# Kernel tuning notes

Hardware: AMD Instinct MI355X
Metric: run time of the kernel (lower is better)

## Reference

```python
import jax, jax.numpy as jnp
import numpy as np

HIDDEN = 256
B, L = 4, 4096


def setup_inputs() -> dict:
    key = jax.random.key(0)
    k_in, k_q, k_k, k_v, k_len = jax.random.split(key, 5)
    inputs = jax.random.normal(k_in, (B, L, HIDDEN), dtype=jnp.float32)
    # torch.rand -> uniform [0,1)
    W_query = jax.random.uniform(k_q, (HIDDEN, HIDDEN), dtype=jnp.float32)
    W_key = jax.random.uniform(k_k, (HIDDEN, HIDDEN), dtype=jnp.float32)
    W_value = jax.random.uniform(k_v, (HIDDEN, HIDDEN), dtype=jnp.float32)
    lengths = jax.random.randint(k_len, (B,), 1, L + 1, dtype=jnp.int64)
    return {"inputs": inputs, "W_query": W_query, "W_key": W_key,
            "W_value": W_value, "lengths": lengths}


def reference(inputs, W_query, W_key, W_value, lengths):
    # lengths is unused by the original module (no masking applied).
    # QKV projections (batched matmul with shared weight)
    queries = jnp.einsum('blh,hd->bld', inputs, W_query)
    keys = jnp.einsum('blh,hd->bld', inputs, W_key)
    values = jnp.einsum('blh,hd->bld', inputs, W_value)
    # scaled dot-product attention, full [B, L, L] scores as in original
    scale = 1.0 / jnp.sqrt(jnp.asarray(HIDDEN, dtype=inputs.dtype))
    attn_scores = jnp.einsum('bqd,bkd->bqk', queries, keys) * scale
    attentions = jax.nn.softmax(attn_scores, axis=-1)
    weighted = jnp.einsum('bqk,bkd->bqd', attentions, values)
    return weighted
```

## Files before the change

### kernel.cpp

```cpp
#include <hip/hip_runtime.h>


typedef __bf16 bf16x8 __attribute__((ext_vector_type(8)));
typedef _Float16 f16x8 __attribute__((ext_vector_type(8)));
typedef _Float16 f16x4 __attribute__((ext_vector_type(4)));
typedef float floatx4 __attribute__((ext_vector_type(4)));

#define MFMA16B(a, b, c) __builtin_amdgcn_mfma_f32_16x16x32_bf16(a, b, c, 0, 0, 0)
#define MFMA16F(a, b, c) __builtin_amdgcn_mfma_f32_16x16x32_f16(a, b, c, 0, 0, 0)
#define GLOAD_LDS16(g, l)                                                  \
  __builtin_amdgcn_global_load_lds(                                        \
      (const __attribute__((address_space(1))) void *)(g),                 \
      (__attribute__((address_space(3))) void *)(l), 16, 0, 0)

#define HID 256
#define LSEQ 4096
#define NB 4
#define NTOK (NB * LSEQ)
#define PLANE ((size_t)NTOK * HID)
#define NSPLIT 4
#define QSCALE 0.09016844005556021f


__device__ __forceinline__ void split_bf16(float v, __bf16 &h, __bf16 &l) {
  h = (__bf16)v;
  l = (__bf16)(v - (float)h);
}

__global__ __launch_bounds__(256) void wsplit(const float *__restrict__ Wq,
                                              const float *__restrict__ Wk,
                                              const float *__restrict__ Wv,
                                              __bf16 *__restrict__ Wht,
                                              __bf16 *__restrict__ Wlt) {
  __shared__ float tile[32][256];
  const int wsel = blockIdx.x;
  const int hb = blockIdx.y;
  const float *W = (wsel == 0) ? Wq : (wsel == 1) ? Wk : Wv;
  __bf16 *oh = Wht + wsel * HID * HID;
  __bf16 *ol = Wlt + wsel * HID * HID;
  const int t = threadIdx.x;
  #pragma unroll
  for (int p = 0; p < 8; ++p) {
    int r = p * 4 + (t >> 6);
    int c = (t & 63) * 4;
    *(floatx4 *)&tile[r][c] = *(const floatx4 *)&W[(hb * 32 + r) * HID + c];
  }
  __syncthreads();
  #pragma unroll
  for (int q = 0; q < 4; ++q) {
    int n = q * 64 + (t >> 2);
    int hs = (t & 3) * 8;
    bf16x8 hh, ll;
    #pragma unroll
    for (int i = 0; i < 8; ++i) {
      float v = tile[hs + i][n];
      __bf16 h, l;
      split_bf16(v, h, l);
      hh[i] = h; ll[i] = l;
    }
    *(bf16x8 *)&oh[n * HID + hb * 32 + hs] = hh;
    *(bf16x8 *)&ol[n * HID + hb * 32 + hs] = ll;
  }
}

__global__ __launch_bounds__(256, 2) void qkv_proj(const float *__restrict__ X,
                                                   const __bf16 *__restrict__ Wht,
                                                   const __bf16 *__restrict__ Wlt,
                                                   _Float16 *__restrict__ Qf,
                                                   _Float16 *__restrict__ Kf,
                                                   _Float16 *__restrict__ Vf) {
  __shared__ __bf16 WhS[64 * 256];
  __shared__ __bf16 WlS[64 * 256];
  _Float16 *Tf = (_Float16 *)WhS;

  const int mtile = blockIdx.x;
  const int col0 = blockIdx.y * 64;
  const int tid = threadIdx.x;
  const int w4 = tid >> 6;
  const int lane = tid & 63;
  const int quad = lane >> 4;
  const int ln = lane & 15;
  const int arow = mtile * 64 + w4 * 16 + ln;

  bf16x8 ah[8], al[8];
  #pragma unroll
  for (int kc = 0; kc < 8; ++kc) {
    const float *xp = X + (size_t)arow * HID + kc * 32 + quad * 8;
    floatx4 x0 = *(const floatx4 *)xp;
    floatx4 x1 = *(const floatx4 *)(xp + 4);
    #pragma unroll
    for (int j = 0; j < 4; ++j) {
      __bf16 h, l;
      split_bf16(x0[j], h, l); ah[kc][j] = h; al[kc][j] = l;
      split_bf16(x1[j], h, l); ah[kc][4 + j] = h; al[kc][4 + j] = l;
    }
  }

  const int srow = tid >> 2;
  const int sseg = tid & 3;

  bf16x8 pwh[8], pwl[8];
  {
    const size_t wbase = (size_t)(col0 + srow) * HID;
    #pragma unroll
    for (int j = 0; j < 8; ++j) {
      const int chunk = j * 4 + sseg;
      pwh[j] = *(const bf16x8 *)&Wht[wbase + chunk * 8];
      pwl[j] = *(const bf16x8 *)&Wlt[wbase + chunk * 8];
    }
  }

  for (int w = 0; w < 3; ++w) {
    __syncthreads();
    #pragma unroll
    for (int j = 0; j < 8; ++j) {
      const int chunk = j * 4 + sseg;
      const int dst = srow * 256 + ((chunk ^ (srow & 7)) << 3);
      *(bf16x8 *)&WhS[dst] = pwh[j];
      if (w < 2) *(bf16x8 *)&WlS[dst] = pwl[j];
    }
    __syncthreads();

    if (w < 2) {
      const size_t wbase = (size_t)(w + 1) * HID * HID + (size_t)(col0 + srow) * HID;
      #pragma unroll
      for (int j = 0; j < 8; ++j) {
        const int chunk = j * 4 + sseg;
        pwh[j] = *(const bf16x8 *)&Wht[wbase + chunk * 8];
        pwl[j] = *(const bf16x8 *)&Wlt[wbase + chunk * 8];
      }
    }

    floatx4 acc[4] = {};
    #pragma unroll
    for (int kc = 0; kc < 8; ++kc) {
      #pragma unroll
      for (int nt = 0; nt < 4; ++nt) {
        const int a = (nt * 16 + ln) * 256 + (((kc * 4 + quad) ^ (ln & 7)) << 3);
        bf16x8 bh = *(const bf16x8 *)&WhS[a];
        acc[nt] = MFMA16B(ah[kc], bh, acc[nt]);
        if (w < 2) {
          bf16x8 bl = *(const bf16x8 *)&WlS[a];
          acc[nt] = MFMA16B(ah[kc], bl, acc[nt]);
        }
        acc[nt] = MFMA16B(al[kc], bh, acc[nt]);
      }
    }

    if (w == 0) {
      #pragma unroll
      for (int nt = 0; nt < 4; ++nt) {
        #pragma unroll
        for (int r = 0; r < 4; ++r) {
          const int orow = mtile * 64 + w4 * 16 + quad * 4 + r;
          const int ocol = col0 + nt * 16 + ln;
          Qf[(size_t)orow * HID + ocol] = (_Float16)(acc[nt][r] * QSCALE);
        }
      }
    } else if (w == 1) {
      __syncthreads();
      #pragma unroll
      for (int nt = 0; nt < 4; ++nt) {
        #pragma unroll
        for (int r = 0; r < 4; ++r) {
          const int tok_l = w4 * 16 + quad * 4 + r;
          const int h_l = nt * 16 + ln;
          Tf[tok_l * 72 + h_l] = (_Float16)acc[nt][r];
        }
      }
      __syncthreads();
      #pragma unroll
      for (int i = 0; i < 2; ++i) {
        const int c = i * 256 + tid;
        const int lane_f = c & 63;
        const int ntf = (c >> 6) & 1;
        const int kcL = (c >> 7) & 1;
        const int t2 = (c >> 8) & 1;
        const int qf = lane_f >> 4;
        const int lnf = lane_f & 15;
        const int tok_l = t2 * 32 + ntf * 16 + lnf;
        f16x8 v = *(const f16x8 *)&Tf[tok_l * 72 + kcL * 32 + qf * 8];
        const int T = mtile * 2 + t2;
        const int kc = (col0 >> 5) + kcL;
        *(f16x8 *)&Kf[(size_t)T * 8192 + ((ntf * 8 + kc) * 64 + lane_f) * 8] = v;
      }
    } else {
      __syncthreads();
      #pragma unroll
      for (int nt = 0; nt < 4; ++nt) {
        #pragma unroll
        for (int r = 0; r < 4; ++r) {
          const int tok_l = w4 * 16 + quad * 4 + r;
          const int d_l = nt * 16 + ln;
          Tf[d_l * 72 + tok_l] = (_Float16)acc[nt][r];
        }
      }
      __syncthreads();
      #pragma unroll
      for (int i = 0; i < 2; ++i) {
        const int c = i * 256 + tid;
        const int lane_f = c & 63;
        const int dtL = (c >> 6) & 3;
        const int t2 = (c >> 8) & 1;
        const int qf = lane_f >> 4;
        const int lnf = lane_f & 15;
        const int d_l = dtL * 16 + lnf;
        f16x4 lo = *(const f16x4 *)&Tf[d_l * 72 + t2 * 32 + 4 * qf];
        f16x4 hi = *(const f16x4 *)&Tf[d_l * 72 + t2 * 32 + 16 + 4 * qf];
        f16x8 v;
        v[0] = lo[0]; v[1] = lo[1]; v[2] = lo[2]; v[3] = lo[3];
        v[4] = hi[0]; v[5] = hi[1]; v[6] = hi[2]; v[7] = hi[3];
        const int T = mtile * 2 + t2;
        const int dt = (col0 >> 4) + dtL;
        *(f16x8 *)&Vf[(size_t)(T * 16 + dt) * 512 + lane_f * 8] = v;
      }
    }
  }
}

__global__ __launch_bounds__(256, 2) void attn(const _Float16 *__restrict__ Qf,
                                               const _Float16 *__restrict__ Kf,
                                               const _Float16 *__restrict__ Vf,
                                               _Float16 *__restrict__ Op,
                                               float *__restrict__ Mp,
                                               float *__restrict__ Lp) {
  __shared__ _Float16 KS[2][8192];
  __shared__ _Float16 VS[2][8192];

  const int bx = blockIdx.x;
  const int ks = bx & 3;
  const int qt = bx >> 2;
  const int b = qt >> 5;
  const int qtl = qt & 31;
  const int tid = threadIdx.x;
  const int w4 = tid >> 6;
  const int lane = tid & 63;
  const int quad = lane >> 4;
  const int ln = lane & 15;
  const int T0 = b * 128 + ks * 32;

  const int qtok0 = b * LSEQ + qtl * 128 + w4 * 16 + ln;
  const int qtok1 = qtok0 + 64;
  f16x8 q0[8], q1[8];
  #pragma unroll
  for (int kc = 0; kc < 8; ++kc) {
    q0[kc] = *(const f16x8 *)&Qf[(size_t)qtok0 * HID + kc * 32 + quad * 8];
    q1[kc] = *(const f16x8 *)&Qf[(size_t)qtok1 * HID + kc * 32 + quad * 8];
  }

  const _Float16 *kuni = Kf + (size_t)T0 * 8192;
  const _Float16 *vuni = Vf + (size_t)T0 * 8192;
  const int koff = tid * 8;
  const int voff = lane * 8;

  #pragma unroll
  for (int i = 0; i < 4; ++i)
    GLOAD_LDS16(kuni + i * 2048 + koff, &KS[0][i * 2048 + koff]);
  #pragma unroll
  for (int i = 0; i < 4; ++i)
    GLOAD_LDS16(vuni + i * 2048 + koff, &VS[0][i * 2048 + koff]);

  float m0 = -1e30f, m1 = -1e30f;
  float l0 = 0.f, l1 = 0.f;
  floatx4 o0[16] = {}, o1[16] = {};

  for (int t = 0; t < 32; ++t) {
    const int buf = t & 1;
    asm volatile("s_waitcnt vmcnt(0)" ::: "memory");
    __builtin_amdgcn_s_barrier();
    __builtin_amdgcn_sched_barrier(0);
    if (t < 31) {
      const _Float16 *ksrc = kuni + (size_t)(t + 1) * 8192 + koff;
      const _Float16 *vsrc = vuni + (size_t)(t + 1) * 8192 + koff;
      #pragma unroll
      for (int i = 0; i < 4; ++i)
        GLOAD_LDS16(ksrc + i * 2048, &KS[buf ^ 1][i * 2048 + koff]);
      #pragma unroll
      for (int i = 0; i < 4; ++i)
        GLOAD_LDS16(vsrc + i * 2048, &VS[buf ^ 1][i * 2048 + koff]);
    }
    const _Float16 *Kb = KS[buf];
    const _Float16 *Vb = VS[buf];

    floatx4 s00, s01, s10, s11;
    {
      floatx4 a00 = {}, b00 = {}, a01 = {}, b01 = {};
      floatx4 a10 = {}, b10 = {}, a11 = {}, b11 = {};
      __builtin_amdgcn_s_setprio(1);
      #pragma unroll
      for (int kc = 0; kc < 4; ++kc) {
        const f16x8 k0 = *(const f16x8 *)(Kb + kc * 512 + voff);
        const f16x8 k1 = *(const f16x8 *)(Kb + (4 + kc) * 512 + voff);
        const f16x8 k2 = *(const f16x8 *)(Kb + (8 + kc) * 512 + voff);
        const f16x8 k3 = *(const f16x8 *)(Kb + (12 + kc) * 512 + voff);
        a00 = MFMA16F(k0, q0[kc], a00);
        a10 = MFMA16F(k0, q1[kc], a10);
        b00 = MFMA16F(k1, q0[4 + kc], b00);
        b10 = MFMA16F(k1, q1[4 + kc], b10);
        a01 = MFMA16F(k2, q0[kc], a01);
        a11 = MFMA16F(k2, q1[kc], a11);
        b01 = MFMA16F(k3, q0[4 + kc], b01);
        b11 = MFMA16F(k3, q1[4 + kc], b11);
      }
      __builtin_amdgcn_s_setprio(0);
      s00 = a00 + b00; s01 = a01 + b01;
      s10 = a10 + b10; s11 = a11 + b11;
    }

    float al0, al1;
    {
      float tmax = fmaxf(fmaxf(fmaxf(s00[0], s00[1]), fmaxf(s00[2], s00[3])),
                         fmaxf(fmaxf(s01[0], s01[1]), fmaxf(s01[2], s01[3])));
      tmax = fmaxf(tmax, __shfl_xor(tmax, 16));
      tmax = fmaxf(tmax, __shfl_xor(tmax, 32));
      const float mn = fmaxf(m0, tmax);
      al0 = exp2f(m0 - mn);
      #pragma unroll
      for (int i = 0; i < 4; ++i) {
        s00[i] = exp2f(s00[i] - mn);
        s01[i] = exp2f(s01[i] - mn);
      }
      float rs = ((s00[0] + s00[1]) + (s00[2] + s00[3])) +
                 ((s01[0] + s01[1]) + (s01[2] + s01[3]));
      rs += __shfl_xor(rs, 16);
      rs += __shfl_xor(rs, 32);
      l0 = l0 * al0 + rs;
      m0 = mn;
    }
    {
      float tmax = fmaxf(fmaxf(fmaxf(s10[0], s10[1]), fmaxf(s10[2], s10[3])),
                         fmaxf(fmaxf(s11[0], s11[1]), fmaxf(s11[2], s11[3])));
      tmax = fmaxf(tmax, __shfl_xor(tmax, 16));
      tmax = fmaxf(tmax, __shfl_xor(tmax, 32));
      const float mn = fmaxf(m1, tmax);
      al1 = exp2f(m1 - mn);
      #pragma unroll
      for (int i = 0; i < 4; ++i) {
        s10[i] = exp2f(s10[i] - mn);
        s11[i] = exp2f(s11[i] - mn);
      }
      float rs = ((s10[0] + s10[1]) + (s10[2] + s10[3])) +
                 ((s11[0] + s11[1]) + (s11[2] + s11[3]));
      rs += __shfl_xor(rs, 16);
      rs += __shfl_xor(rs, 32);
      l1 = l1 * al1 + rs;
      m1 = mn;
    }

    f16x8 pf0, pf1;
    pf0[0] = (_Float16)s00[0]; pf0[1] = (_Float16)s00[1];
    pf0[2] = (_Float16)s00[2]; pf0[3] = (_Float16)s00[3];
    pf0[4] = (_Float16)s01[0]; pf0[5] = (_Float16)s01[1];
    pf0[6] = (_Float16)s01[2]; pf0[7] = (_Float16)s01[3];
    pf1[0] = (_Float16)s10[0]; pf1[1] = (_Float16)s10[1];
    pf1[2] = (_Float16)s10[2]; pf1[3] = (_Float16)s10[3];
    pf1[4] = (_Float16)s11[0]; pf1[5] = (_Float16)s11[1];
    pf1[6] = (_Float16)s11[2]; pf1[7] = (_Float16)s11[3];

    if (__any(al0 < 1.0f)) {
      #pragma unroll
      for (int dt = 0; dt < 16; ++dt) {
        o0[dt][0] *= al0; o0[dt][1] *= al0; o0[dt][2] *= al0; o0[dt][3] *= al0;
      }
    }
    if (__any(al1 < 1.0f)) {
      #pragma unroll
      for (int dt = 0; dt < 16; ++dt) {
        o1[dt][0] *= al1; o1[dt][1] *= al1; o1[dt][2] *= al1; o1[dt][3] *= al1;
      }
    }

    __builtin_amdgcn_s_setprio(1);
    #pragma unroll
    for (int dt = 0; dt < 16; ++dt) {
      const f16x8 vf = *(const f16x8 *)(Vb + dt * 512 + voff);
      o0[dt] = MFMA16F(vf, pf0, o0[dt]);
      o1[dt] = MFMA16F(vf, pf1, o1[dt]);
    }
    __builtin_amdgcn_s_setprio(0);
    __builtin_amdgcn_sched_barrier(0);
  }

  #pragma unroll
  for (int dt = 0; dt < 16; ++dt) {
    f16x4 v4;
    v4[0] = (_Float16)o0[dt][0]; v4[1] = (_Float16)o0[dt][1];
    v4[2] = (_Float16)o0[dt][2]; v4[3] = (_Float16)o0[dt][3];
    *(f16x4 *)&Op[(size_t)ks * PLANE + (size_t)qtok0 * HID + dt * 16 + quad * 4] = v4;
    f16x4 w4v;
    w4v[0] = (_Float16)o1[dt][0]; w4v[1] = (_Float16)o1[dt][1];
    w4v[2] = (_Float16)o1[dt][2]; w4v[3] = (_Float16)o1[dt][3];
    *(f16x4 *)&Op[(size_t)ks * PLANE + (size_t)qtok1 * HID + dt * 16 + quad * 4] = w4v;
  }
  if (quad == 0) {
    Mp[ks * NTOK + qtok0] = m0;
    Lp[ks * NTOK + qtok0] = l0;
    Mp[ks * NTOK + qtok1] = m1;
    Lp[ks * NTOK + qtok1] = l1;
  }
}

__global__ __launch_bounds__(256) void merge(const _Float16 *__restrict__ Op,
                                             const float *__restrict__ Mp,
                                             const float *__restrict__ Lp,
                                             float *__restrict__ Out) {
  const int row = blockIdx.x * 4 + (threadIdx.x >> 6);
  const int c = (threadIdx.x & 63) * 4;
  float ms[NSPLIT], ls[NSPLIT];
  #pragma unroll
  for (int s = 0; s < NSPLIT; ++s) {
    ms[s] = Mp[s * NTOK + row];
    ls[s] = Lp[s * NTOK + row];
  }
  const float M = fmaxf(fmaxf(ms[0], ms[1]), fmaxf(ms[2], ms[3]));
  float e[NSPLIT], den = 0.f;
  #pragma unroll
  for (int s = 0; s < NSPLIT; ++s) {
    e[s] = exp2f(ms[s] - M);
    den += ls[s] * e[s];
  }
  const float inv = 1.0f / den;
  floatx4 out = {};
  #pragma unroll
  for (int s = 0; s < NSPLIT; ++s) {
    const f16x4 a = *(const f16x4 *)&Op[(size_t)s * PLANE + (size_t)row * HID + c];
    const float w = e[s] * inv;
    #pragma unroll
    for (int i = 0; i < 4; ++i) out[i] += w * (float)a[i];
  }
  *(floatx4 *)&Out[(size_t)row * HID + c] = out;
}

extern "C" void kernel_launch(void *const *d_in, const int *in_sizes, int n_in,
                              void *d_out, int out_size, void *d_ws, size_t ws_size,
                              hipStream_t stream) {
  const float *X = (const float *)d_in[0];
  const float *Wq = (const float *)d_in[1];
  const float *Wk = (const float *)d_in[2];
  const float *Wv = (const float *)d_in[3];

  _Float16 *ws = (_Float16 *)d_ws;
  _Float16 *Qf = ws;
  _Float16 *Kf = Qf + PLANE;
  _Float16 *Vf = Kf + PLANE;
  __bf16 *Wht = (__bf16 *)(Vf + PLANE);
  __bf16 *Wlt = Wht + 3 * HID * HID;
  _Float16 *Op = (_Float16 *)(Wlt + 3 * HID * HID);
  float *Mp = (float *)(Op + NSPLIT * PLANE);
  float *Lp = Mp + NSPLIT * NTOK;

  wsplit<<<dim3(3, 8), 256, 0, stream>>>(Wq, Wk, Wv, Wht, Wlt);
  qkv_proj<<<dim3(256, 4), 256, 0, stream>>>(X, Wht, Wlt, Qf, Kf, Vf);
  attn<<<NTOK / 128 * NSPLIT, 256, 0, stream>>>(Qf, Kf, Vf, Op, Mp, Lp);
  merge<<<NTOK / 4, 256, 0, stream>>>(Op, Mp, Lp, (float *)d_out);
}
```

Measured before the change: 206.7 us.

## Process 128 rows per block in QKV projection to reuse staged weights

Each qkv_proj block now handles two 64-row token tiles, so every weight tile staged in shared memory feeds twice as many MFMAs, and the grid is halved. The register prefetch of the next weight matrix is dropped in favor of loading each matrix at the top of its loop iteration. The transpose buffer gets its own shared allocation, raising LDS use to about 73 KB and register pressure from doubled A fragments and accumulators, which may hurt occupancy under the launch bound of 2. The projection is a small part of total time next to attention.

After: 202.3 us. 1.02x faster.

```diff
diff --git a/kernel.cpp b/kernel.cpp
--- a/kernel.cpp
+++ b/kernel.cpp
@@ -71,7 +71,7 @@
                                                    _Float16 *__restrict__ Vf) {
   __shared__ __bf16 WhS[64 * 256];
   __shared__ __bf16 WlS[64 * 256];
-  _Float16 *Tf = (_Float16 *)WhS;
+  __shared__ _Float16 Tf[64 * 72];
 
   const int mtile = blockIdx.x;
   const int col0 = blockIdx.y * 64;
@@ -80,70 +80,76 @@
   const int lane = tid & 63;
   const int quad = lane >> 4;
   const int ln = lane & 15;
-  const int arow = mtile * 64 + w4 * 16 + ln;
-
-  bf16x8 ah[8], al[8];
+  const int arow0 = mtile * 128 + w4 * 16 + ln;
+  const int arow1 = arow0 + 64;
+
+  bf16x8 ah0[8], al0[8], ah1[8], al1[8];
   #pragma unroll
   for (int kc = 0; kc < 8; ++kc) {
-    const float *xp = X + (size_t)arow * HID + kc * 32 + quad * 8;
-    floatx4 x0 = *(const floatx4 *)xp;
-    floatx4 x1 = *(const floatx4 *)(xp + 4);
-    #pragma unroll
-    for (int j = 0; j < 4; ++j) {
-      __bf16 h, l;
-      split_bf16(x0[j], h, l); ah[kc][j] = h; al[kc][j] = l;
-      split_bf16(x1[j], h, l); ah[kc][4 + j] = h; al[kc][4 + j] = l;
+    {
+      const float *xp = X + (size_t)arow0 * HID + kc * 32 + quad * 8;
+      floatx4 x0 = *(const floatx4 *)xp;
+      floatx4 x1 = *(const floatx4 *)(xp + 4);
+      #pragma unroll
+      for (int j = 0; j < 4; ++j) {
+        __bf16 h, l;
+        split_bf16(x0[j], h, l); ah0[kc][j] = h; al0[kc][j] = l;
+        split_bf16(x1[j], h, l); ah0[kc][4 + j] = h; al0[kc][4 + j] = l;
+      }
+    }
+    {
+      const float *xp = X + (size_t)arow1 * HID + kc * 32 + quad * 8;
+      floatx4 x0 = *(const floatx4 *)xp;
+      floatx4 x1 = *(const floatx4 *)(xp + 4);
+      #pragma unroll
+      for (int j = 0; j < 4; ++j) {
+        __bf16 h, l;
+        split_bf16(x0[j], h, l); ah1[kc][j] = h; al1[kc][j] = l;
+        split_bf16(x1[j], h, l); ah1[kc][4 + j] = h; al1[kc][4 + j] = l;
+      }
     }
   }
 
   const int srow = tid >> 2;
   const int sseg = tid & 3;
 
-  bf16x8 pwh[8], pwl[8];
-  {
-    const size_t wbase = (size_t)(col0 + srow) * HID;
-    #pragma unroll
-    for (int j = 0; j < 8; ++j) {
-      const int chunk = j * 4 + sseg;
-      pwh[j] = *(const bf16x8 *)&Wht[wbase + chunk * 8];
-      pwl[j] = *(const bf16x8 *)&Wlt[wbase + chunk * 8];
-    }
-  }
-
   for (int w = 0; w < 3; ++w) {
+    bf16x8 th[8], tl[8];
+    {
+      const size_t wbase = (size_t)w * HID * HID + (size_t)(col0 + srow) * HID;
+      #pragma unroll
+      for (int j = 0; j < 8; ++j) {
+        const int chunk = j * 4 + sseg;
+        th[j] = *(const bf16x8 *)&Wht[wbase + chunk * 8];
+        if (w < 2) tl[j] = *(const bf16x8 *)&Wlt[wbase + chunk * 8];
+      }
+    }
     __syncthreads();
     #pragma unroll
     for (int j = 0; j < 8; ++j) {
       const int chunk = j * 4 + sseg;
       const int dst = srow * 256 + ((chunk ^ (srow & 7)) << 3);
-      *(bf16x8 *)&WhS[dst] = pwh[j];
-      if (w < 2) *(bf16x8 *)&WlS[dst] = pwl[j];
+      *(bf16x8 *)&WhS[dst] = th[j];
+      if (w < 2) *(bf16x8 *)&WlS[dst] = tl[j];
     }
     __syncthreads();
 
-    if (w < 2) {
-      const size_t wbase = (size_t)(w + 1) * HID * HID + (size_t)(col0 + srow) * HID;
-      #pragma unroll
-      for (int j = 0; j < 8; ++j) {
-        const int chunk = j * 4 + sseg;
-        pwh[j] = *(const bf16x8 *)&Wht[wbase + chunk * 8];
-        pwl[j] = *(const bf16x8 *)&Wlt[wbase + chunk * 8];
-      }
-    }
-
-    floatx4 acc[4] = {};
+    floatx4 acc0[4] = {}, acc1[4] = {};
     #pragma unroll
     for (int kc = 0; kc < 8; ++kc) {
       #pragma unroll
       for (int nt = 0; nt < 4; ++nt) {
         const int a = (nt * 16 + ln) * 256 + (((kc * 4 + quad) ^ (ln & 7)) << 3);
         bf16x8 bh = *(const bf16x8 *)&WhS[a];
-        acc[nt] = MFMA16B(ah[kc], bh, acc[nt]);
+        acc0[nt] = MFMA16B(ah0[kc], bh, acc0[nt]);
+        acc1[nt] = MFMA16B(ah1[kc], bh, acc1[nt]);
         if (w < 2) {
           bf16x8 bl = *(const bf16x8 *)&WlS[a];
-          acc[nt] = MFMA16B(ah[kc], bl, acc[nt]);
-        }
-        acc[nt] = MFMA16B(al[kc], bh, acc[nt]);
+          acc0[nt] = MFMA16B(ah0[kc], bl, acc0[nt]);
+          acc1[nt] = MFMA16B(ah1[kc], bl, acc1[nt]);
+        }
+        acc0[nt] = MFMA16B(al0[kc], bh, acc0[nt]);
+        acc1[nt] = MFMA16B(al1[kc], bh, acc1[nt]);
       }
     }
 
@@ -152,67 +158,74 @@
       for (int nt = 0; nt < 4; ++nt) {
         #pragma unroll
         for (int r = 0; r < 4; ++r) {
-          const int orow = mtile * 64 + w4 * 16 + quad * 4 + r;
+          const int orow = mtile * 128 + w4 * 16 + quad * 4 + r;
           const int ocol = col0 + nt * 16 + ln;
-          Qf[(size_t)orow * HID + ocol] = (_Float16)(acc[nt][r] * QSCALE);
+          Qf[(size_t)orow * HID + ocol] = (_Float16)(acc0[nt][r] * QSCALE);
+          Qf[(size_t)(orow + 64) * HID + ocol] = (_Float16)(acc1[nt][r] * QSCALE);
         }
       }
     } else if (w == 1) {
-      __syncthreads();
-      #pragma unroll
-      for (int nt = 0; nt < 4; ++nt) {
+      #pragma unroll
+      for (int h = 0; h < 2; ++h) {
         #pragma unroll
-        for (int r = 0; r < 4; ++r) {
-          const int tok_l = w4 * 16 + quad * 4 + r;
-          const int h_l = nt * 16 + ln;
-          Tf[tok_l * 72 + h_l] = (_Float16)acc[nt][r];
-        }
-      }
-      __syncthreads();
-      #pragma unroll
-      for (int i = 0; i < 2; ++i) {
-        const int c = i * 256 + tid;
-        const int lane_f = c & 63;
-        const int ntf = (c >> 6) & 1;
-        const int kcL = (c >> 7) & 1;
-        const int t2 = (c >> 8) & 1;
-        const int qf = lane_f >> 4;
-        const int lnf = lane_f & 15;
-        const int tok_l = t2 * 32 + ntf * 16 + lnf;
-        f16x8 v = *(const f16x8 *)&Tf[tok_l * 72 + kcL * 32 + qf * 8];
-        const int T = mtile * 2 + t2;
-        const int kc = (col0 >> 5) + kcL;
-        *(f16x8 *)&Kf[(size_t)T * 8192 + ((ntf * 8 + kc) * 64 + lane_f) * 8] = v;
+        for (int nt = 0; nt < 4; ++nt) {
+          #pragma unroll
+          for (int r = 0; r < 4; ++r) {
+            const int tok_l = w4 * 16 + quad * 4 + r;
+            const int h_l = nt * 16 + ln;
+            Tf[tok_l * 72 + h_l] = (_Float16)((h == 0 ? acc0 : acc1)[nt][r]);
+          }
+        }
+        __syncthreads();
+        #pragma unroll
+        for (int i = 0; i < 2; ++i) {
+          const int c = i * 256 + tid;
+          const int lane_f = c & 63;
+          const int ntf = (c >> 6) & 1;
+          const int kcL = (c >> 7) & 1;
+          const int t2 = (c >> 8) & 1;
+          const int qf = lane_f >> 4;
+          const int lnf = lane_f & 15;
+          const int tok_l = t2 * 32 + ntf * 16 + lnf;
+          f16x8 v = *(const f16x8 *)&Tf[tok_l * 72 + kcL * 32 + qf * 8];
+          const int T = mtile * 4 + h * 2 + t2;
+          const int kc2 = (col0 >> 5) + kcL;
+          *(f16x8 *)&Kf[(size_t)T * 8192 + ((ntf * 8 + kc2) * 64 + lane_f) * 8] = v;
+        }
+        __syncthreads();
       }
     } else {
-      __syncthreads();
-      #pragma unroll
-      for (int nt = 0; nt < 4; ++nt) {
+      #pragma unroll
+      for (int h = 0; h < 2; ++h) {
         #pragma unroll
-        for (int r = 0; r < 4; ++r) {
-          const int tok_l = w4 * 16 + quad * 4 + r;
-          const int d_l = nt * 16 + ln;
-          Tf[d_l * 72 + tok_l] = (_Float16)acc[nt][r];
-        }
-      }
-      __syncthreads();
-      #pragma unroll
-      for (int i = 0; i < 2; ++i) {
-        const int c = i * 256 + tid;
-        const int lane_f = c & 63;
-        const int dtL = (c >> 6) & 3;
-        const int t2 = (c >> 8) & 1;
-        const int qf = lane_f >> 4;
-        const int lnf = lane_f & 15;
-        const int d_l = dtL * 16 + lnf;
-        f16x4 lo = *(const f16x4 *)&Tf[d_l * 72 + t2 * 32 + 4 * qf];
-        f16x4 hi = *(const f16x4 *)&Tf[d_l * 72 + t2 * 32 + 16 + 4 * qf];
-        f16x8 v;
-        v[0] = lo[0]; v[1] = lo[1]; v[2] = lo[2]; v[3] = lo[3];
-        v[4] = hi[0]; v[5] = hi[1]; v[6] = hi[2]; v[7] = hi[3];
-        const int T = mtile * 2 + t2;
-        const int dt = (col0 >> 4) + dtL;
-        *(f16x8 *)&Vf[(size_t)(T * 16 + dt) * 512 + lane_f * 8] = v;
+        for (int nt = 0; nt < 4; ++nt) {
+          #pragma unroll
+          for (int r = 0; r < 4; ++r) {
+            const int tok_l = w4 * 16 + quad * 4 + r;
+            const int d_l = nt * 16 + ln;
+            Tf[d_l * 72 + tok_l] = (_Float16)((h == 0 ? acc0 : acc1)[nt][r]);
+          }
+        }
+        __syncthreads();
+        #pragma unroll
+        for (int i = 0; i < 2; ++i) {
+          const int c = i * 256 + tid;
+          const int lane_f = c & 63;
+          const int dtL = (c >> 6) & 3;
+          const int t2 = (c >> 8) & 1;
+          const int qf = lane_f >> 4;
+          const int lnf = lane_f & 15;
+          const int d_l = dtL * 16 + lnf;
+          f16x4 lo = *(const f16x4 *)&Tf[d_l * 72 + t2 * 32 + 4 * qf];
+          f16x4 hi = *(const f16x4 *)&Tf[d_l * 72 + t2 * 32 + 16 + 4 * qf];
+          f16x8 v;
+          v[0] = lo[0]; v[1] = lo[1]; v[2] = lo[2]; v[3] = lo[3];
+          v[4] = hi[0]; v[5] = hi[1]; v[6] = hi[2]; v[7] = hi[3];
+          const int T = mtile * 4 + h * 2 + t2;
+          const int dt = (col0 >> 4) + dtL;
+          *(f16x8 *)&Vf[(size_t)(T * 16 + dt) * 512 + lane_f * 8] = v;
+        }
+        __syncthreads();
       }
     }
   }
@@ -450,7 +463,7 @@
   float *Lp = Mp + NSPLIT * NTOK;
 
   wsplit<<<dim3(3, 8), 256, 0, stream>>>(Wq, Wk, Wv, Wht, Wlt);
-  qkv_proj<<<dim3(256, 4), 256, 0, stream>>>(X, Wht, Wlt, Qf, Kf, Vf);
+  qkv_proj<<<dim3(128, 4), 256, 0, stream>>>(X, Wht, Wlt, Qf, Kf, Vf);
   attn<<<NTOK / 128 * NSPLIT, 256, 0, stream>>>(Qf, Kf, Vf, Op, Mp, Lp);
   merge<<<NTOK / 4, 256, 0, stream>>>(Op, Mp, Lp, (float *)d_out);
 }
```
